# Optimization experiments

Hardware: AMD Instinct MI355X
Metric: run time of the kernel (lower is better)

## Reference

```python
import jax, jax.numpy as jnp
import numpy as np

B, S, D = 8, 2048, 256


def setup_inputs() -> dict:
    key = jax.random.key(0)
    ks = jax.random.split(key, 8)
    nodes = jax.random.normal(ks[0], (B, S, D), dtype=jnp.float32)
    mask = jax.random.randint(ks[1], (B, S), 0, 2, dtype=jnp.int32)
    # ensure at least one unmasked position per row to avoid all--inf softmax
    mask = mask.at[:, 0].set(1)
    scale = 1.0 / np.sqrt(D)
    Wq = jax.random.normal(ks[2], (D, D), dtype=jnp.float32) * scale
    bq = jnp.zeros((D,), dtype=jnp.float32)
    Wk = jax.random.normal(ks[3], (D, D), dtype=jnp.float32) * scale
    bk = jnp.zeros((D,), dtype=jnp.float32)
    Wv = jax.random.normal(ks[4], (D, D), dtype=jnp.float32) * scale
    bv = jnp.zeros((D,), dtype=jnp.float32)
    return {"nodes": nodes, "mask": mask, "Wq": Wq, "bq": bq,
            "Wk": Wk, "bk": bk, "Wv": Wv, "bv": bv}


def reference(nodes, mask, Wq, bq, Wk, bk, Wv, bv):
    # Linear layers: x @ W.T + b (torch nn.Linear convention)
    q = jnp.einsum('bsd,ed->bse', nodes, Wq) + bq   # [B,S,D]
    k = jnp.einsum('bsd,ed->bse', nodes, Wk) + bk
    v = jnp.einsum('bsd,ed->bse', nodes, Wv) + bv
    d = k.shape[-1]
    scores = jnp.einsum('bqd,bkd->bqk', q, k) / jnp.sqrt(jnp.float32(d))  # [B,S,S]
    # mask[b, j] == 0 masks key column j for every query row
    scores = jnp.where(mask[:, None, :] != 0, scores, -jnp.inf)
    attn = jax.nn.softmax(scores, axis=-1)           # [B,S,S]
    weighted = jnp.einsum('bqk,bkd->bqd', attn, v)   # [B,S,D]
    return jnp.mean(weighted, axis=1)                # [B,D]
```

## Files before the change

### kernel.cpp

```cpp
#include <hip/hip_runtime.h>
#include <hip/hip_bf16.h>
#include <stdint.h>


typedef short short8 __attribute__((ext_vector_type(8)));
typedef float floatx4 __attribute__((ext_vector_type(4)));
typedef float floatx2 __attribute__((ext_vector_type(2)));

#define MFMA16(a, b, c) __builtin_amdgcn_mfma_f32_16x16x32_bf16((a), (b), (c), 0, 0, 0)

#define ASYNC16(gsrc, ldst)                                                    \
    __builtin_amdgcn_global_load_lds(                                          \
        (__attribute__((address_space(1))) void*)(void*)(gsrc),                \
        (__attribute__((address_space(3))) void*)(ldst), 16, 0, 0)

static __device__ __forceinline__ unsigned short f2bf(float f) {
    union { float f; unsigned u; } v; v.f = f;
    unsigned r = v.u + 0x7fffu + ((v.u >> 16) & 1u);
    return (unsigned short)(r >> 16);
}
static __device__ __forceinline__ float bf2f(unsigned short h) {
    union { unsigned u; float f; } v; v.u = ((unsigned)h) << 16;
    return v.f;
}

__global__ __launch_bounds__(256) void k_cc(
    const float* __restrict__ nodes, const float* __restrict__ Wq,
    const float* __restrict__ Wk, const float* __restrict__ Wv,
    unsigned short* __restrict__ nbf, unsigned short* __restrict__ wbf,
    const int* __restrict__ mask, int* __restrict__ cidx, int* __restrict__ cnt,
    int* __restrict__ slot_of ,
    unsigned short* __restrict__ kbt,
    float* __restrict__ zbase ,
    float* __restrict__ outp )
{
    int blk = blockIdx.x;
    if (blk < 2144) {
        int unit = blk * 256 + threadIdx.x;
        const float* src;
        unsigned short* dst;
        int off;
        if (unit < 524288) {
            src = nodes; dst = nbf; off = unit * 8;
        } else {
            int j = (unit - 524288) * 8;
            int m = j >> 16;
            int r = j & 65535;
            src = (m == 0) ? Wq : (m == 1 ? Wk : Wv);
            dst = wbf + m * 65536;
            off = r;
        }
        float4 a = *(const float4*)(src + off);
        float4 b = *(const float4*)(src + off + 4);
        short8 o;
        o[0] = f2bf(a.x); o[1] = f2bf(a.y); o[2] = f2bf(a.z); o[3] = f2bf(a.w);
        o[4] = f2bf(b.x); o[5] = f2bf(b.y); o[6] = f2bf(b.z); o[7] = f2bf(b.w);
        *(short8*)(dst + off) = o;
        return;
    }
    if (blk < 2152) {
        if (threadIdx.x < 64) {
            int b = blk - 2144, lane = threadIdx.x;
            int base = 0;
            for (int c = 0; c < 2048; c += 64) {
                int m = mask[b * 2048 + c + lane];
                unsigned long long bal = __ballot(m != 0);
                int pre = __popcll(bal & ((1ull << lane) - 1ull));
                if (m) {
                    cidx[b * 2048 + base + pre] = c + lane;
                    slot_of[b * 2048 + c + lane] = base + pre;
                } else {
                    slot_of[b * 2048 + c + lane] = -1;
                }
                base += __popcll(bal);
            }
            if (lane == 0) cnt[b] = base;
            for (int i = base + lane; i < 2048; i += 64) cidx[b * 2048 + i] = 0;
            int cntPad = (base + 63) & ~63;
            int pad = cntPad - base;
            short8 z8 = {};
            for (int i = lane; i < pad * 32; i += 64) {
                int slot = base + (i >> 5);
                int du = i & 31;
                size_t off = ((size_t)b * 32 + (slot >> 6)) * 16384
                           + ((size_t)du * 64 + (slot & 63)) * 8;
                *(short8*)(kbt + off) = z8;
            }
        }
        return;
    }
    int idx = (blk - 2152) * 256 + threadIdx.x;
    float4 z = {0.f, 0.f, 0.f, 0.f};
#pragma unroll
    for (int j = 0; j < 2; ++j) {
        int p = idx + j * 4352;
        if (p < 8192) ((float4*)zbase)[p] = z;
        else ((float4*)outp)[p - 8192] = z;
    }
}

__global__ __launch_bounds__(256) void k_proj2b(
    const unsigned short* __restrict__ nbf,
    const unsigned short* __restrict__ wbf,
    const float* __restrict__ bq, const float* __restrict__ bk,
    const float* __restrict__ bv,
    const int* __restrict__ slot_of,
    unsigned short* __restrict__ qb, unsigned short* __restrict__ kbt,
    unsigned short* __restrict__ vb)
{
    __shared__ __align__(16) unsigned short As[128 * 64];
    __shared__ __align__(16) unsigned short Bs[128 * 64];
    int tid = threadIdx.x, lane = tid & 63, wave = tid >> 6;
    int wm = wave & 1, wn = wave >> 1;
    int l15 = lane & 15, quad = lane >> 4;
    int mBase = blockIdx.x * 128;
    int nBase = blockIdx.y * 128;
    int z = blockIdx.z;
    const unsigned short* W = wbf + z * 65536;

    floatx4 acc[4][4] = {};

    for (int kc = 0; kc < 256; kc += 64) {
#pragma unroll
        for (int i = 0; i < 4; ++i) {
            int p = i * 256 + wave * 64 + lane;
            int row = p >> 3;
            int col8 = (p & 7) ^ (row & 7);
            int goff = row * 256 + kc + col8 * 8;
            unsigned short* dstA = &As[(i * 256 + wave * 64) * 8];
            unsigned short* dstB = &Bs[(i * 256 + wave * 64) * 8];
            ASYNC16(nbf + mBase * 256 + goff, dstA);
            ASYNC16(W + nBase * 256 + goff, dstB);
        }
        __syncthreads();
#pragma unroll
        for (int ks = 0; ks < 2; ++ks) {
            int c8 = ks * 4 + quad;
            short8 af[4], bfr[4];
#pragma unroll
            for (int i = 0; i < 4; ++i) {
                int row = wm * 64 + i * 16 + l15;
                af[i] = *(const short8*)(&As[(row * 8 + (c8 ^ (row & 7))) * 8]);
            }
#pragma unroll
            for (int i = 0; i < 4; ++i) {
                int row = wn * 64 + i * 16 + l15;
                bfr[i] = *(const short8*)(&Bs[(row * 8 + (c8 ^ (row & 7))) * 8]);
            }
#pragma unroll
            for (int mi = 0; mi < 4; ++mi)
#pragma unroll
                for (int ni = 0; ni < 4; ++ni)
                    acc[mi][ni] = MFMA16(af[mi], bfr[ni], acc[mi][ni]);
        }
        __syncthreads();
    }

    const float* bias = (z == 0) ? bq : (z == 1 ? bk : bv);
    float scale = (z == 0) ? 0.0625f : 1.0f;
    if (z == 1) {
#pragma unroll
        for (int mi = 0; mi < 4; ++mi)
#pragma unroll
            for (int ni = 0; ni < 4; ++ni) {
                int col = nBase + wn * 64 + ni * 16 + l15;
                float bval = bias[col];
                int du = col >> 3, cj = col & 7;
#pragma unroll
                for (int r = 0; r < 4; ++r) {
                    int row = mBase + wm * 64 + mi * 16 + quad * 4 + r;
                    int slot = slot_of[row];
                    if (slot >= 0) {
                        int b = row >> 11;
                        size_t off = ((size_t)b * 32 + (slot >> 6)) * 16384
                                   + ((size_t)du * 64 + (slot & 63)) * 8 + cj;
                        kbt[off] = f2bf(acc[mi][ni][r] + bval);
                    }
                }
            }
    } else {
        unsigned short* out = (z == 0) ? qb : vb;
#pragma unroll
        for (int mi = 0; mi < 4; ++mi)
#pragma unroll
            for (int ni = 0; ni < 4; ++ni) {
                int col = nBase + wn * 64 + ni * 16 + l15;
                float bval = bias[col];
#pragma unroll
                for (int r = 0; r < 4; ++r) {
                    int row = mBase + wm * 64 + mi * 16 + quad * 4 + r;
                    out[row * 256 + col] = f2bf((acc[mi][ni][r] + bval) * scale);
                }
            }
    }
}

__global__ __launch_bounds__(256) void k_pass1v(
    const unsigned short* __restrict__ qb, const unsigned short* __restrict__ kbt,
    const int* __restrict__ cnt_g, float* __restrict__ lsum_g,
    unsigned char* __restrict__ pbuf)
{
    __shared__ __align__(16) unsigned short kt[16384];
    int tid = threadIdx.x, lane = tid & 63, wave = tid >> 6;
    int l15 = lane & 15, quad = lane >> 4;
    int b = blockIdx.z;
    int cnt = cnt_g[b];
    int nchunk = (cnt + 63) >> 6;
    int qBase = blockIdx.x * 128 + wave * 32;
    int qcg = blockIdx.x * 4 + wave;

    short8 qf[2][8];
#pragma unroll
    for (int mi = 0; mi < 2; ++mi)
#pragma unroll
        for (int ks = 0; ks < 8; ++ks)
            qf[mi][ks] = *(const short8*)(qb + (b * 2048 + qBase + mi * 16 + l15) * 256 + ks * 32 + quad * 8);

    float ls[2][4] = {};
    for (int c = blockIdx.y; c < nchunk; c += 4) {
        const unsigned short* src = kbt + ((size_t)b * 32 + c) * 16384;
#pragma unroll
        for (int i = 0; i < 8; ++i) {
            int seg = wave * 8 + i;
            ASYNC16(src + seg * 512 + lane * 8, &kt[seg * 512]);
        }
        __syncthreads();
#pragma unroll
        for (int nt = 0; nt < 4; ++nt) {
            short8 kf[8];
#pragma unroll
            for (int ks = 0; ks < 8; ++ks)
                kf[ks] = *(const short8*)(&kt[((ks * 4 + quad) * 64 + nt * 16 + l15) * 8]);
            floatx4 acc[2] = {};
#pragma unroll
            for (int ks = 0; ks < 8; ++ks) {
                acc[0] = MFMA16(qf[0][ks], kf[ks], acc[0]);
                acc[1] = MFMA16(qf[1][ks], kf[ks], acc[1]);
            }
            float bias = (c * 64 + nt * 16 + l15 < cnt) ? 0.0f : -1e30f;
            float e[2][4];
#pragma unroll
            for (int mi = 0; mi < 2; ++mi)
#pragma unroll
                for (int r = 0; r < 4; ++r) {
                    e[mi][r] = __expf(acc[mi][r] + bias);
                    ls[mi][r] += e[mi][r];
                }
            int ktile = c * 4 + nt;
            if (ktile < 96) {
                int w0 = __builtin_amdgcn_cvt_pk_fp8_f32(e[0][0], e[0][1], 0, 0);
                w0 = __builtin_amdgcn_cvt_pk_fp8_f32(e[0][2], e[0][3], w0, 1);
                int w1 = __builtin_amdgcn_cvt_pk_fp8_f32(e[1][0], e[1][1], 0, 0);
                w1 = __builtin_amdgcn_cvt_pk_fp8_f32(e[1][2], e[1][3], w1, 1);
                size_t off = ((((size_t)b * 96 + ktile) * 64 + qcg) * 64 + lane) * 8;
                uint2 pv; pv.x = (unsigned)w0; pv.y = (unsigned)w1;
                *(uint2*)(pbuf + off) = pv;
            }
        }
        __syncthreads();
    }
#pragma unroll
    for (int mi = 0; mi < 2; ++mi)
#pragma unroll
        for (int r = 0; r < 4; ++r) {
            float v = ls[mi][r];
            v += __shfl_xor(v, 1); v += __shfl_xor(v, 2);
            v += __shfl_xor(v, 4); v += __shfl_xor(v, 8);
            if (l15 == 0)
                atomicAdd(&lsum_g[b * 2048 + qBase + mi * 16 + quad * 4 + r], v);
        }
}

__global__ __launch_bounds__(512) void k_wred5(
    const unsigned char* __restrict__ pbuf, const float* __restrict__ lsum_g,
    const int* __restrict__ cidx, const int* __restrict__ cnt_g,
    float* __restrict__ wsum_g)
{
    __shared__ float linv_p[2048];
    int tid = threadIdx.x, lane = tid & 63, wave = tid >> 6;
    int l15 = lane & 15, quad = lane >> 4;
    int b = blockIdx.z;
    int ktile = blockIdx.y * 8 + wave;

#pragma unroll
    for (int i = 0; i < 4; ++i) {
        int idx = i * 512 + tid;
        int qcg = idx >> 5, qd = (idx >> 3) & 3, j = idx & 7;
        int q = qcg * 32 + (j >> 2) * 16 + qd * 4 + (j & 3);
        linv_p[idx] = 1.0f / lsum_g[b * 2048 + q];
    }
    __syncthreads();

    int cnt = cnt_g[b];
    if (ktile >= 96 || ktile * 16 >= cnt) return;

    int qcg0 = blockIdx.x * 32;
    float acc = 0.f;
#pragma unroll 4
    for (int qcg = qcg0; qcg < qcg0 + 32; ++qcg) {
        size_t off = ((((size_t)b * 96 + ktile) * 64 + qcg) * 64 + lane) * 8;
        uint2 pv = *(const uint2*)(pbuf + off);
        const float* lv = &linv_p[(qcg * 4 + quad) * 8];
        floatx2 p01 = __builtin_amdgcn_cvt_pk_f32_fp8(pv.x, 0);
        floatx2 p23 = __builtin_amdgcn_cvt_pk_f32_fp8(pv.x, 1);
        floatx2 p45 = __builtin_amdgcn_cvt_pk_f32_fp8(pv.y, 0);
        floatx2 p67 = __builtin_amdgcn_cvt_pk_f32_fp8(pv.y, 1);
        acc += p01[0] * lv[0] + p01[1] * lv[1] + p23[0] * lv[2] + p23[1] * lv[3]
             + p45[0] * lv[4] + p45[1] * lv[5] + p67[0] * lv[6] + p67[1] * lv[7];
    }
    acc += __shfl_xor(acc, 16);
    acc += __shfl_xor(acc, 32);
    int slot = ktile * 16 + l15;
    if (lane < 16 && slot < cnt)
        atomicAdd(&wsum_g[b * 2048 + cidx[b * 2048 + slot]], acc);
}

__global__ __launch_bounds__(256) void k_out(
    const float* __restrict__ wsum_g, const unsigned short* __restrict__ vb,
    float* __restrict__ outp)
{
    int b = blockIdx.y;
    int d = threadIdx.x;
    int k0 = blockIdx.x * 128;
    float acc = 0.f;
#pragma unroll 4
    for (int k = k0; k < k0 + 128; ++k) {
        float wv = wsum_g[b * 2048 + k];
        acc += wv * bf2f(vb[(b * 2048 + k) * 256 + d]);
    }
    atomicAdd(&outp[b * 256 + d], acc * (1.0f / 2048.0f));
}

extern "C" void kernel_launch(void* const* d_in, const int* in_sizes, int n_in,
                              void* d_out, int out_size, void* d_ws, size_t ws_size,
                              hipStream_t stream)
{
    const float* nodes = (const float*)d_in[0];
    const int*   mask  = (const int*)d_in[1];
    const float* Wq    = (const float*)d_in[2];
    const float* bq    = (const float*)d_in[3];
    const float* Wk    = (const float*)d_in[4];
    const float* bk    = (const float*)d_in[5];
    const float* Wv    = (const float*)d_in[6];
    const float* bv    = (const float*)d_in[7];
    float* out = (float*)d_out;

    unsigned short* qb  = (unsigned short*)d_ws;
    unsigned short* vb  = qb + 4194304;
    float* lsum = (float*)(vb + 4194304);
    float* wsum = lsum + 16384;
    int*   cnt  = (int*)(wsum + 16384);
    int*   cidx = cnt + 16;
    int*   slot_of = cidx + 16384;
    unsigned short* kbt = (unsigned short*)(slot_of + 16384);
    unsigned short* X   = kbt + 4194304;
    unsigned short* nbf = X;
    unsigned short* wbf = X + 4194304;
    unsigned char* pbuf = (unsigned char*)X;

    k_cc<<<2169, 256, 0, stream>>>(nodes, Wq, Wk, Wv, nbf, wbf,
                                   mask, cidx, cnt, slot_of, kbt, lsum, out);
    k_proj2b<<<dim3(128, 2, 3), 256, 0, stream>>>(nbf, wbf, bq, bk, bv,
                                                  slot_of, qb, kbt, vb);
    k_pass1v<<<dim3(16, 4, 8), 256, 0, stream>>>(qb, kbt, cnt, lsum, pbuf);
    k_wred5<<<dim3(2, 16, 8), 512, 0, stream>>>(pbuf, lsum, cidx, cnt, wsum);
    k_out<<<dim3(16, 8), 256, 0, stream>>>(wsum, vb, out);
}
```

Before: 142.8 us.

## Fuse key-weight reduction with V output, store V compacted by unmasked slot

The V projection now writes only unmasked rows into a compacted buffer indexed by slot, which removes the cidx index buffer and the wsum scatter. The weight-reduction kernel and the output kernel are merged into one 1024-thread kernel. It reduces the per-key softmax weights into shared memory and immediately accumulates weight times V for its 128 compacted slots before atomically adding into the output. This removes one launch, the wsum global round trip and the zeroing of wsum, at the cost of fewer, larger blocks (96 total) and more output atomics per batch.

New measurement: 134.6 us. 5.7% less time.

```diff
diff --git a/kernel.cpp b/kernel.cpp
--- a/kernel.cpp
+++ b/kernel.cpp
@@ -28,7 +28,7 @@
     const float* __restrict__ nodes, const float* __restrict__ Wq,
     const float* __restrict__ Wk, const float* __restrict__ Wv,
     unsigned short* __restrict__ nbf, unsigned short* __restrict__ wbf,
-    const int* __restrict__ mask, int* __restrict__ cidx, int* __restrict__ cnt,
+    const int* __restrict__ mask, int* __restrict__ cnt,
     int* __restrict__ slot_of ,
     unsigned short* __restrict__ kbt,
     float* __restrict__ zbase ,
@@ -66,16 +66,10 @@
                 int m = mask[b * 2048 + c + lane];
                 unsigned long long bal = __ballot(m != 0);
                 int pre = __popcll(bal & ((1ull << lane) - 1ull));
-                if (m) {
-                    cidx[b * 2048 + base + pre] = c + lane;
-                    slot_of[b * 2048 + c + lane] = base + pre;
-                } else {
-                    slot_of[b * 2048 + c + lane] = -1;
-                }
+                slot_of[b * 2048 + c + lane] = m ? (base + pre) : -1;
                 base += __popcll(bal);
             }
             if (lane == 0) cnt[b] = base;
-            for (int i = base + lane; i < 2048; i += 64) cidx[b * 2048 + i] = 0;
             int cntPad = (base + 63) & ~63;
             int pad = cntPad - base;
             short8 z8 = {};
@@ -91,12 +85,8 @@
     }
     int idx = (blk - 2152) * 256 + threadIdx.x;
     float4 z = {0.f, 0.f, 0.f, 0.f};
-#pragma unroll
-    for (int j = 0; j < 2; ++j) {
-        int p = idx + j * 4352;
-        if (p < 8192) ((float4*)zbase)[p] = z;
-        else ((float4*)outp)[p - 8192] = z;
-    }
+    if (idx < 4096) ((float4*)zbase)[idx] = z;
+    else ((float4*)outp)[idx - 4096] = z;
 }
 
 __global__ __launch_bounds__(256) void k_proj2b(
@@ -106,7 +96,7 @@
     const float* __restrict__ bv,
     const int* __restrict__ slot_of,
     unsigned short* __restrict__ qb, unsigned short* __restrict__ kbt,
-    unsigned short* __restrict__ vb)
+    unsigned short* __restrict__ vbc)
 {
     __shared__ __align__(16) unsigned short As[128 * 64];
     __shared__ __align__(16) unsigned short Bs[128 * 64];
@@ -157,7 +147,6 @@
     }
 
     const float* bias = (z == 0) ? bq : (z == 1 ? bk : bv);
-    float scale = (z == 0) ? 0.0625f : 1.0f;
     if (z == 1) {
 #pragma unroll
         for (int mi = 0; mi < 4; ++mi)
@@ -178,8 +167,7 @@
                     }
                 }
             }
-    } else {
-        unsigned short* out = (z == 0) ? qb : vb;
+    } else if (z == 2) {
 #pragma unroll
         for (int mi = 0; mi < 4; ++mi)
 #pragma unroll
@@ -189,7 +177,26 @@
 #pragma unroll
                 for (int r = 0; r < 4; ++r) {
                     int row = mBase + wm * 64 + mi * 16 + quad * 4 + r;
-                    out[row * 256 + col] = f2bf((acc[mi][ni][r] + bval) * scale);
+                    int slot = slot_of[row];
+                    if (slot >= 0) {
+                        int b = row >> 11;
+                        vbc[((size_t)b * 2048 + slot) * 256 + col] =
+                            f2bf(acc[mi][ni][r] + bval);
+                    }
+                }
+            }
+    } else {
+        float scale = 0.0625f;
+#pragma unroll
+        for (int mi = 0; mi < 4; ++mi)
+#pragma unroll
+            for (int ni = 0; ni < 4; ++ni) {
+                int col = nBase + wn * 64 + ni * 16 + l15;
+                float bval = bias[col];
+#pragma unroll
+                for (int r = 0; r < 4; ++r) {
+                    int row = mBase + wm * 64 + mi * 16 + quad * 4 + r;
+                    qb[row * 256 + col] = f2bf((acc[mi][ni][r] + bval) * scale);
                 }
             }
     }
@@ -271,20 +278,24 @@
         }
 }
 
-__global__ __launch_bounds__(512) void k_wred5(
+__global__ __launch_bounds__(1024) void k_wo(
     const unsigned char* __restrict__ pbuf, const float* __restrict__ lsum_g,
-    const int* __restrict__ cidx, const int* __restrict__ cnt_g,
-    float* __restrict__ wsum_g)
+    const int* __restrict__ cnt_g, const unsigned short* __restrict__ vbc,
+    float* __restrict__ outp)
 {
     __shared__ float linv_p[2048];
-    int tid = threadIdx.x, lane = tid & 63, wave = tid >> 6;
+    __shared__ float w2_s[2][128];
+    __shared__ float o_s[1024];
+    int tid = threadIdx.x, lane = tid & 63;
     int l15 = lane & 15, quad = lane >> 4;
-    int b = blockIdx.z;
-    int ktile = blockIdx.y * 8 + wave;
-
-#pragma unroll
-    for (int i = 0; i < 4; ++i) {
-        int idx = i * 512 + tid;
+    int b = blockIdx.y;
+    int kt = (tid >> 6) & 7;
+    int qh = tid >> 9;
+    int ktile = blockIdx.x * 8 + kt;
+
+#pragma unroll
+    for (int i = 0; i < 2; ++i) {
+        int idx = i * 1024 + tid;
         int qcg = idx >> 5, qd = (idx >> 3) & 3, j = idx & 7;
         int q = qcg * 32 + (j >> 2) * 16 + qd * 4 + (j & 3);
         linv_p[idx] = 1.0f / lsum_g[b * 2048 + q];
@@ -292,43 +303,47 @@
     __syncthreads();
 
     int cnt = cnt_g[b];
-    if (ktile >= 96 || ktile * 16 >= cnt) return;
-
-    int qcg0 = blockIdx.x * 32;
     float acc = 0.f;
+    if (ktile * 16 < cnt) {
+        int qcg0 = qh * 32;
 #pragma unroll 4
-    for (int qcg = qcg0; qcg < qcg0 + 32; ++qcg) {
-        size_t off = ((((size_t)b * 96 + ktile) * 64 + qcg) * 64 + lane) * 8;
-        uint2 pv = *(const uint2*)(pbuf + off);
-        const float* lv = &linv_p[(qcg * 4 + quad) * 8];
-        floatx2 p01 = __builtin_amdgcn_cvt_pk_f32_fp8(pv.x, 0);
-        floatx2 p23 = __builtin_amdgcn_cvt_pk_f32_fp8(pv.x, 1);
-        floatx2 p45 = __builtin_amdgcn_cvt_pk_f32_fp8(pv.y, 0);
-        floatx2 p67 = __builtin_amdgcn_cvt_pk_f32_fp8(pv.y, 1);
-        acc += p01[0] * lv[0] + p01[1] * lv[1] + p23[0] * lv[2] + p23[1] * lv[3]
-             + p45[0] * lv[4] + p45[1] * lv[5] + p67[0] * lv[6] + p67[1] * lv[7];
+        for (int qcg = qcg0; qcg < qcg0 + 32; ++qcg) {
+            size_t off = ((((size_t)b * 96 + ktile) * 64 + qcg) * 64 + lane) * 8;
+            uint2 pv = *(const uint2*)(pbuf + off);
+            const float* lv = &linv_p[(qcg * 4 + quad) * 8];
+            floatx2 p01 = __builtin_amdgcn_cvt_pk_f32_fp8(pv.x, 0);
+            floatx2 p23 = __builtin_amdgcn_cvt_pk_f32_fp8(pv.x, 1);
+            floatx2 p45 = __builtin_amdgcn_cvt_pk_f32_fp8(pv.y, 0);
+            floatx2 p67 = __builtin_amdgcn_cvt_pk_f32_fp8(pv.y, 1);
+            acc += p01[0] * lv[0] + p01[1] * lv[1] + p23[0] * lv[2] + p23[1] * lv[3]
+                 + p45[0] * lv[4] + p45[1] * lv[5] + p67[0] * lv[6] + p67[1] * lv[7];
+        }
     }
     acc += __shfl_xor(acc, 16);
     acc += __shfl_xor(acc, 32);
     int slot = ktile * 16 + l15;
-    if (lane < 16 && slot < cnt)
-        atomicAdd(&wsum_g[b * 2048 + cidx[b * 2048 + slot]], acc);
-}
-
-__global__ __launch_bounds__(256) void k_out(
-    const float* __restrict__ wsum_g, const unsigned short* __restrict__ vb,
-    float* __restrict__ outp)
-{
-    int b = blockIdx.y;
-    int d = threadIdx.x;
-    int k0 = blockIdx.x * 128;
-    float acc = 0.f;
+    if (lane < 16)
+        w2_s[qh][kt * 16 + l15] = (slot < cnt) ? acc : 0.f;
+    __syncthreads();
+
+    int d = tid & 255, quarter = tid >> 8;
+    float oacc = 0.f;
+    int s0 = quarter * 32;
 #pragma unroll 4
-    for (int k = k0; k < k0 + 128; ++k) {
-        float wv = wsum_g[b * 2048 + k];
-        acc += wv * bf2f(vb[(b * 2048 + k) * 256 + d]);
-    }
-    atomicAdd(&outp[b * 256 + d], acc * (1.0f / 2048.0f));
+    for (int j = 0; j < 32; ++j) {
+        int sl = s0 + j;
+        float w = w2_s[0][sl] + w2_s[1][sl];
+        if (w != 0.f) {
+            int sg = blockIdx.x * 128 + sl;
+            oacc += w * bf2f(vbc[((size_t)b * 2048 + sg) * 256 + d]);
+        }
+    }
+    o_s[tid] = oacc;
+    __syncthreads();
+    if (tid < 256) {
+        float t = o_s[tid] + o_s[tid + 256] + o_s[tid + 512] + o_s[tid + 768];
+        atomicAdd(&outp[b * 256 + tid], t * (1.0f / 2048.0f));
+    }
 }
 
 extern "C" void kernel_launch(void* const* d_in, const int* in_sizes, int n_in,
@@ -345,24 +360,21 @@
     const float* bv    = (const float*)d_in[7];
     float* out = (float*)d_out;
 
-    unsigned short* qb  = (unsigned short*)d_ws;
-    unsigned short* vb  = qb + 4194304;
-    float* lsum = (float*)(vb + 4194304);
-    float* wsum = lsum + 16384;
-    int*   cnt  = (int*)(wsum + 16384);
-    int*   cidx = cnt + 16;
-    int*   slot_of = cidx + 16384;
+    unsigned short* qb   = (unsigned short*)d_ws;
+    unsigned short* vbc  = qb + 4194304;
+    float* lsum = (float*)(vbc + 4194304);
+    int*   cnt  = (int*)(lsum + 16384);
+    int*   slot_of = cnt + 16;
     unsigned short* kbt = (unsigned short*)(slot_of + 16384);
     unsigned short* X   = kbt + 4194304;
     unsigned short* nbf = X;
     unsigned short* wbf = X + 4194304;
     unsigned char* pbuf = (unsigned char*)X;
 
-    k_cc<<<2169, 256, 0, stream>>>(nodes, Wq, Wk, Wv, nbf, wbf,
-                                   mask, cidx, cnt, slot_of, kbt, lsum, out);
+    k_cc<<<2170, 256, 0, stream>>>(nodes, Wq, Wk, Wv, nbf, wbf,
+                                   mask, cnt, slot_of, kbt, lsum, out);
     k_proj2b<<<dim3(128, 2, 3), 256, 0, stream>>>(nbf, wbf, bq, bk, bv,
-                                                  slot_of, qb, kbt, vb);
+                                                  slot_of, qb, kbt, vbc);
     k_pass1v<<<dim3(16, 4, 8), 256, 0, stream>>>(qb, kbt, cnt, lsum, pbuf);
-    k_wred5<<<dim3(2, 16, 8), 512, 0, stream>>>(pbuf, lsum, cidx, cnt, wsum);
-    k_out<<<dim3(16, 8), 256, 0, stream>>>(wsum, vb, out);
-}
+    k_wo<<<dim3(12, 8), 1024, 0, stream>>>(pbuf, lsum, cnt, vbc, out);
+}
```
